# Performance work log

Hardware: AMD Instinct MI355X
Metric: run time of the kernel (lower is better)

The kernel has to match this reference:

```python
import jax, jax.numpy as jnp
import numpy as np

HID = 128      # hidden_dim
HEADS = 8      # num_heads
PHD = 16       # per_head_dim
NTYPES = 3     # num_edge_types
N = 50000      # num nodes
E = 250000     # edges per edge type


def setup_inputs() -> dict:
    key = jax.random.key(0)
    ks = jax.random.split(key, 8)
    x = jax.random.normal(ks[0], (N, HID), dtype=jnp.float32)
    adj0 = jax.random.randint(ks[1], (E, 2), 0, N)
    adj1 = jax.random.randint(ks[2], (E, 2), 0, N)
    adj2 = jax.random.randint(ks[3], (E, 2), 0, N)
    # weights stored [in, out] so application is x @ W (same math as torch Linear)
    Wq = jax.random.normal(ks[4], (NTYPES, HID, HEADS * PHD), dtype=jnp.float32) * 0.05
    Wk = jax.random.normal(ks[5], (NTYPES, HID, HEADS * PHD), dtype=jnp.float32) * 0.05
    Wm = jax.random.normal(ks[6], (NTYPES, 2 * HID, HEADS * PHD), dtype=jnp.float32) * 0.05
    bm = jax.random.normal(ks[7], (NTYPES, HEADS * PHD), dtype=jnp.float32) * 0.01
    return {"x": x, "adj0": adj0, "adj1": adj1, "adj2": adj2,
            "Wq": Wq, "Wk": Wk, "Wm": Wm, "bm": bm}


def reference(x, adj0, adj1, adj2, Wq, Wk, Wm, bm):
    scale = PHD ** (-0.5)
    n = x.shape[0]
    msgs, scores, tgts = [], [], []
    for t, adj in enumerate((adj0, adj1, adj2)):
        src_r = x[adj[:, 0]]                       # [E, HID]
        tgt_r = x[adj[:, 1]]                       # [E, HID]
        pair = jnp.concatenate([src_r, tgt_r], axis=1)      # [E, 2*HID]
        m = jax.nn.relu(pair @ Wm[t] + bm[t]).reshape(-1, HEADS, PHD)
        q = (tgt_r @ Wq[t]).reshape(-1, HEADS, PHD) * scale
        k = (src_r @ Wk[t]).reshape(-1, HEADS, PHD)
        s = jnp.einsum('ehd,ehd->eh', q, k)        # [E, HEADS]
        msgs.append(m); scores.append(s); tgts.append(adj[:, 1])
    all_m = jnp.concatenate(msgs, axis=0)          # [TE, HEADS, PHD]
    all_s = jnp.concatenate(scores, axis=0)        # [TE, HEADS]
    all_t = jnp.concatenate(tgts, axis=0)          # [TE]
    # segment log-softmax over edges grouped by target node
    smax = jax.ops.segment_max(all_s, all_t, num_segments=n)        # [N, HEADS]
    shifted = all_s - smax[all_t]
    sumexp = jax.ops.segment_sum(jnp.exp(shifted), all_t, num_segments=n)
    logZ = jnp.log(jnp.where(sumexp > 0, sumexp, 1.0))
    probs = jnp.exp(shifted - logZ[all_t])                          # [TE, HEADS]
    agg = jax.ops.segment_sum(probs[..., None] * all_m, all_t, num_segments=n)
    return agg.reshape(n, HEADS * PHD)
```

## Files before the change

### kernel.cpp

```cpp
#include <hip/hip_runtime.h>

#define HID 128
#define NE 250000
#define NT 3
#define NN 50000
#define CAP 48
#define PLANE (NN * 256)
#define GEMM_BLOCKS 391
#define EDGE_BLOCKS ((NT * NE + 255) / 256)

typedef unsigned int u32;
typedef unsigned short u16;
typedef __attribute__((ext_vector_type(8))) short short8;
typedef __attribute__((ext_vector_type(4))) float f32x4;

__device__ __forceinline__ u16 f2bf(float f) {
    u32 u = __float_as_uint(f);
    u += 0x7fffu + ((u >> 16) & 1u);
    return (u16)(u >> 16);
}
__device__ __forceinline__ float bflo(u32 u) { return __uint_as_float(u << 16); }
__device__ __forceinline__ float bfhi(u32 u) { return __uint_as_float(u & 0xffff0000u); }

__device__ __forceinline__ short8 pack8(const float4 a, const float4 b) {
    short8 r;
    r[0] = (short)f2bf(a.x); r[1] = (short)f2bf(a.y);
    r[2] = (short)f2bf(a.z); r[3] = (short)f2bf(a.w);
    r[4] = (short)f2bf(b.x); r[5] = (short)f2bf(b.y);
    r[6] = (short)f2bf(b.z); r[7] = (short)f2bf(b.w);
    return r;
}

__global__ __launch_bounds__(256)
void init_kernel(const float* __restrict__ Wq, const float* __restrict__ Wk,
                 const float* __restrict__ Wm,
                 u16* __restrict__ Wtb, u32* __restrict__ counts)
{
    const int b = blockIdx.x, tid = threadIdx.x;
    if (b < 768) {
        const int gid = b * 256 + tid;
        const int mat = gid >> 14;
        const int i   = gid & 16383;
        const int k   = i >> 7;
        const int n   = i & 127;
        const int t   = mat >> 2;
        const int m   = mat & 3;
        const float* src;
        if (m == 0)      src = Wq + (size_t)t * 16384;
        else if (m == 1) src = Wk + (size_t)t * 16384;
        else if (m == 2) src = Wm + (size_t)t * 32768;
        else             src = Wm + (size_t)t * 32768 + 16384;
        Wtb[(size_t)mat * 16384 + n * HID + k] = f2bf(src[i]);
    } else {
        const int gid = (b - 768) * 256 + tid;
        if (gid < NN / 4) {
            uint4 z; z.x = 0u; z.y = 0u; z.z = 0u; z.w = 0u;
            ((uint4*)counts)[gid] = z;
        }
    }
}

__global__ __launch_bounds__(256)
void big_kernel(const float* __restrict__ x, const u16* __restrict__ Wtb,
                const float* __restrict__ bm,
                const int* __restrict__ a0, const int* __restrict__ a1,
                const int* __restrict__ a2,
                u32* __restrict__ counts, u32* __restrict__ edata,
                u16* __restrict__ P)
{
    const int b = blockIdx.x;
    const int tid = threadIdx.x;

    if (b >= GEMM_BLOCKS) {
        const int gid = (b - GEMM_BLOCKS) * 256 + tid;
        if (gid < NT * NE) {
            const int t = gid / NE, e = gid - t * NE;
            const int* adj = (t == 0) ? a0 : (t == 1) ? a1 : a2;
            const int2 pr = ((const int2*)adj)[e];
            const u32 pos = atomicAdd(&counts[pr.y], 1u);
            if (pos < CAP)
                edata[(size_t)pr.y * CAP + pos] = (u32)pr.x | ((u32)t << 16);
        }
        return;
    }

    const int wave = tid >> 6, lane = tid & 63;
    const int lm = lane & 15, quad = lane >> 4;
    const int r0 = b * 128 + wave * 32;
    const int ar0 = min(r0 + lm,      NN - 1);
    const int ar1 = min(r0 + 16 + lm, NN - 1);

    short8 Xf0[4], Xf1[4];
    #pragma unroll
    for (int ki = 0; ki < 4; ++ki) {
        const float* xp0 = x + (size_t)ar0 * HID + ki * 32 + quad * 8;
        const float* xp1 = x + (size_t)ar1 * HID + ki * 32 + quad * 8;
        Xf0[ki] = pack8(*(const float4*)xp0, *(const float4*)(xp0 + 4));
        Xf1[ki] = pack8(*(const float4*)xp1, *(const float4*)(xp1 + 4));
    }

    for (int mat = 0; mat < 12; ++mat) {
        const int t = mat >> 2, m = mat & 3;
        const u16* Wf0 = Wtb + (size_t)mat * 16384 + lm * HID + quad * 8;

        f32x4 acc[8][2];
        #pragma unroll
        for (int ct = 0; ct < 8; ++ct) {
            acc[ct][0] = (f32x4){0.f, 0.f, 0.f, 0.f};
            acc[ct][1] = (f32x4){0.f, 0.f, 0.f, 0.f};
        }
        #pragma unroll
        for (int ki = 0; ki < 4; ++ki) {
            #pragma unroll
            for (int ct = 0; ct < 8; ++ct) {
                const short8 Wf = *(const short8*)(Wf0 + ct * 16 * HID + ki * 32);
                acc[ct][0] = __builtin_amdgcn_mfma_f32_16x16x32_bf16(Wf, Xf0[ki], acc[ct][0], 0, 0, 0);
                acc[ct][1] = __builtin_amdgcn_mfma_f32_16x16x32_bf16(Wf, Xf1[ki], acc[ct][1], 0, 0, 0);
            }
        }

        const int half = (m >= 2) ? 128 : 0;
        const int pidx = (m == 1 || m == 2) ? t : (3 + t);
        u16* Pd = P + (size_t)pidx * PLANE + half;
        #pragma unroll
        for (int ct = 0; ct < 8; ++ct) {
            const int oc = ct * 16 + quad * 4;
            float b0 = 0.f, b1 = 0.f, b2 = 0.f, b3 = 0.f;
            if (m == 3) {
                const float4 bv = *(const float4*)(bm + t * HID + oc);
                b0 = bv.x; b1 = bv.y; b2 = bv.z; b3 = bv.w;
            }
            #pragma unroll
            for (int nt = 0; nt < 2; ++nt) {
                const int node = r0 + nt * 16 + lm;
                if (node < NN) {
                    uint2 pk;
                    pk.x = (u32)f2bf(acc[ct][nt][0] + b0) | ((u32)f2bf(acc[ct][nt][1] + b1) << 16);
                    pk.y = (u32)f2bf(acc[ct][nt][2] + b2) | ((u32)f2bf(acc[ct][nt][3] + b3) << 16);
                    *(uint2*)(Pd + (size_t)node * 256 + oc) = pk;
                }
            }
        }
    }
}

__global__ __launch_bounds__(256)
void gather_kernel(const u16* __restrict__ P, const u32* __restrict__ counts,
                   const u32* __restrict__ edata, float* __restrict__ out)
{
    const int wave = threadIdx.x >> 6, lane = threadIdx.x & 63;
    const int node = blockIdx.x * 4 + wave;
    if (node >= NN) return;
    const int j0 = lane * 2;

    const int dg = min((int)__builtin_amdgcn_readfirstlane((int)counts[node]), CAP);
    const int idxs = (lane < CAP) ? (int)edata[(size_t)node * CAP + lane] : 0;

    float q0[NT], q1[NT], b0[NT], b1[NT];
    #pragma unroll
    for (int t = 0; t < NT; ++t) {
        const u16* qb = P + (size_t)(3 + t) * PLANE + (size_t)node * 256;
        const u32 qv = *(const u32*)(qb + j0);
        const u32 bv = *(const u32*)(qb + 128 + j0);
        q0[t] = bflo(qv) * 0.25f;
        q1[t] = bfhi(qv) * 0.25f;
        b0[t] = bflo(bv);
        b1[t] = bfhi(bv);
    }

    float acc0 = 0.f, acc1 = 0.f, den = 0.f;
    for (int e = 0; e < dg; e += 16) {
        u32 kv[16], av[16];
        int ty[16];
        #pragma unroll
        for (int u = 0; u < 16; ++u) {
            int w = __builtin_amdgcn_readlane(idxs, e + u);
            w = (e + u < dg) ? w : 0;
            w = __builtin_amdgcn_readfirstlane(w);
            const int tt = w >> 16, s = w & 0xffff;
            ty[u] = tt;
            const u16* ka = P + (size_t)tt * PLANE + (size_t)s * 256;
            kv[u] = *(const u32*)(ka + j0);
            av[u] = *(const u32*)(ka + 128 + j0);
        }
        #pragma unroll
        for (int u = 0; u < 16; ++u) {
            const int tt = ty[u];
            const float cq0 = (tt == 0) ? q0[0] : (tt == 1) ? q0[1] : q0[2];
            const float cq1 = (tt == 0) ? q1[0] : (tt == 1) ? q1[1] : q1[2];
            const float cb0 = (tt == 0) ? b0[0] : (tt == 1) ? b0[1] : b0[2];
            const float cb1 = (tt == 0) ? b1[0] : (tt == 1) ? b1[1] : b1[2];
            float d = cq0 * bflo(kv[u]) + cq1 * bfhi(kv[u]);
            d += __shfl_xor(d, 1);
            d += __shfl_xor(d, 2);
            d += __shfl_xor(d, 4);
            float ex = __expf(d);
            ex = (e + u < dg) ? ex : 0.f;
            den  += ex;
            acc0 += ex * fmaxf(bflo(av[u]) + cb0, 0.f);
            acc1 += ex * fmaxf(bfhi(av[u]) + cb1, 0.f);
        }
    }

    const float inv = den > 0.f ? 1.f / den : 0.f;
    float2 o;
    o.x = acc0 * inv;
    o.y = acc1 * inv;
    *(float2*)(out + (size_t)node * HID + j0) = o;
}

extern "C" void kernel_launch(void* const* d_in, const int* in_sizes, int n_in,
                              void* d_out, int out_size, void* d_ws, size_t ws_size,
                              hipStream_t stream)
{
    const float* x  = (const float*)d_in[0];
    const int* a0   = (const int*)d_in[1];
    const int* a1   = (const int*)d_in[2];
    const int* a2   = (const int*)d_in[3];
    const float* Wq = (const float*)d_in[4];
    const float* Wk = (const float*)d_in[5];
    const float* Wm = (const float*)d_in[6];
    const float* bm = (const float*)d_in[7];
    float* out = (float*)d_out;

    const size_t planeB = (size_t)PLANE * sizeof(u16);
    char* p = (char*)d_ws;
    u16* P      = (u16*)p;  p += 6 * planeB;
    u16* Wtb    = (u16*)p;  p += 393216;
    u32* counts = (u32*)p;  p += 200000;
    u32* edata  = (u32*)p;

    init_kernel<<<768 + 49, 256, 0, stream>>>(Wq, Wk, Wm, Wtb, counts);
    big_kernel<<<GEMM_BLOCKS + EDGE_BLOCKS, 256, 0, stream>>>(
        x, Wtb, bm, a0, a1, a2, counts, edata, P);
    gather_kernel<<<(NN + 3) / 4, 256, 0, stream>>>(P, counts, edata, out);
}
```

Baseline: 267.3 us.

## Split GEMM work across waves by weight matrix with 16-node blocks

Each GEMM block now handles 16 nodes instead of 128, and its four waves each compute three of the twelve weight matrices rather than every wave computing all twelve for its own 32 nodes. This takes the block count from 391 to 3125, which fills the GPU better and cuts per-wave register pressure, with launch bounds set to ask for 4 blocks per SM. In exchange, each x row is loaded and converted redundantly by all four waves, and each MFMA reuses a weight fragment across 16 nodes instead of 32, which doubles weight traffic per node. NN divides evenly by 16, so the bounds checks can be dropped.

New measurement: 331.9 us. 24.2% more time.

```diff
diff --git a/kernel.cpp b/kernel.cpp
--- a/kernel.cpp
+++ b/kernel.cpp
@@ -6,7 +6,7 @@
 #define NN 50000
 #define CAP 48
 #define PLANE (NN * 256)
-#define GEMM_BLOCKS 391
+#define GEMM_BLOCKS 3125
 #define EDGE_BLOCKS ((NT * NE + 255) / 256)
 
 typedef unsigned int u32;
@@ -60,7 +60,7 @@
     }
 }
 
-__global__ __launch_bounds__(256)
+__global__ __launch_bounds__(256, 4)
 void big_kernel(const float* __restrict__ x, const u16* __restrict__ Wtb,
                 const float* __restrict__ bm,
                 const int* __restrict__ a0, const int* __restrict__ a1,
@@ -86,42 +86,36 @@
 
     const int wave = tid >> 6, lane = tid & 63;
     const int lm = lane & 15, quad = lane >> 4;
-    const int r0 = b * 128 + wave * 32;
-    const int ar0 = min(r0 + lm,      NN - 1);
-    const int ar1 = min(r0 + 16 + lm, NN - 1);
-
-    short8 Xf0[4], Xf1[4];
+    const int node = b * 16 + lm;
+
+    short8 Xf[4];
     #pragma unroll
     for (int ki = 0; ki < 4; ++ki) {
-        const float* xp0 = x + (size_t)ar0 * HID + ki * 32 + quad * 8;
-        const float* xp1 = x + (size_t)ar1 * HID + ki * 32 + quad * 8;
-        Xf0[ki] = pack8(*(const float4*)xp0, *(const float4*)(xp0 + 4));
-        Xf1[ki] = pack8(*(const float4*)xp1, *(const float4*)(xp1 + 4));
-    }
-
-    for (int mat = 0; mat < 12; ++mat) {
+        const float* xp = x + (size_t)node * HID + ki * 32 + quad * 8;
+        Xf[ki] = pack8(*(const float4*)xp, *(const float4*)(xp + 4));
+    }
+
+    #pragma unroll 1
+    for (int i = 0; i < 3; ++i) {
+        const int mat = wave * 3 + i;
         const int t = mat >> 2, m = mat & 3;
         const u16* Wf0 = Wtb + (size_t)mat * 16384 + lm * HID + quad * 8;
 
-        f32x4 acc[8][2];
-        #pragma unroll
-        for (int ct = 0; ct < 8; ++ct) {
-            acc[ct][0] = (f32x4){0.f, 0.f, 0.f, 0.f};
-            acc[ct][1] = (f32x4){0.f, 0.f, 0.f, 0.f};
-        }
+        f32x4 acc[8];
+        #pragma unroll
+        for (int ct = 0; ct < 8; ++ct) acc[ct] = (f32x4){0.f, 0.f, 0.f, 0.f};
         #pragma unroll
         for (int ki = 0; ki < 4; ++ki) {
             #pragma unroll
             for (int ct = 0; ct < 8; ++ct) {
                 const short8 Wf = *(const short8*)(Wf0 + ct * 16 * HID + ki * 32);
-                acc[ct][0] = __builtin_amdgcn_mfma_f32_16x16x32_bf16(Wf, Xf0[ki], acc[ct][0], 0, 0, 0);
-                acc[ct][1] = __builtin_amdgcn_mfma_f32_16x16x32_bf16(Wf, Xf1[ki], acc[ct][1], 0, 0, 0);
+                acc[ct] = __builtin_amdgcn_mfma_f32_16x16x32_bf16(Wf, Xf[ki], acc[ct], 0, 0, 0);
             }
         }
 
         const int half = (m >= 2) ? 128 : 0;
         const int pidx = (m == 1 || m == 2) ? t : (3 + t);
-        u16* Pd = P + (size_t)pidx * PLANE + half;
+        u16* Pd = P + (size_t)pidx * PLANE + half + (size_t)node * 256;
         #pragma unroll
         for (int ct = 0; ct < 8; ++ct) {
             const int oc = ct * 16 + quad * 4;
@@ -130,16 +124,10 @@
                 const float4 bv = *(const float4*)(bm + t * HID + oc);
                 b0 = bv.x; b1 = bv.y; b2 = bv.z; b3 = bv.w;
             }
-            #pragma unroll
-            for (int nt = 0; nt < 2; ++nt) {
-                const int node = r0 + nt * 16 + lm;
-                if (node < NN) {
-                    uint2 pk;
-                    pk.x = (u32)f2bf(acc[ct][nt][0] + b0) | ((u32)f2bf(acc[ct][nt][1] + b1) << 16);
-                    pk.y = (u32)f2bf(acc[ct][nt][2] + b2) | ((u32)f2bf(acc[ct][nt][3] + b3) << 16);
-                    *(uint2*)(Pd + (size_t)node * 256 + oc) = pk;
-                }
-            }
+            uint2 pk;
+            pk.x = (u32)f2bf(acc[ct][0] + b0) | ((u32)f2bf(acc[ct][1] + b1) << 16);
+            pk.y = (u32)f2bf(acc[ct][2] + b2) | ((u32)f2bf(acc[ct][3] + b3) << 16);
+            *(uint2*)(Pd + oc) = pk;
         }
     }
 }
```

## Stage GEMM weight tiles in double-buffered swizzled LDS with register prefetch

Applied to the files above, without the earlier changes.

Each GEMM block now copies each 128x128 bf16 weight matrix into shared memory, using an XOR swizzle so bank conflicts are avoided, and the MFMA loop reads its weight fragments from LDS instead of global memory. The next matrix is prefetched into registers during the current matrix's compute and written to the other LDS buffer, followed by a barrier. This removes the redundant per-wave global and L2 traffic for weights, since four waves previously each reloaded every matrix. In exchange it adds 64KB of LDS per block, which may reduce occupancy, plus extra staging registers and one barrier per matrix. The edge-binning blocks launched from the same kernel also have to reserve this LDS allocation.

Measured after the change: 224.8 us. 1.19x faster.

```diff
diff --git a/kernel.cpp b/kernel.cpp
--- a/kernel.cpp
+++ b/kernel.cpp
@@ -68,6 +68,7 @@
                 u32* __restrict__ counts, u32* __restrict__ edata,
                 u16* __restrict__ P)
 {
+    __shared__ u16 Ws[2][128 * 128];
     const int b = blockIdx.x;
     const int tid = threadIdx.x;
 
@@ -99,9 +100,32 @@
         Xf1[ki] = pack8(*(const float4*)xp1, *(const float4*)(xp1 + 4));
     }
 
+    {
+        short8 stg[8];
+        #pragma unroll
+        for (int i = 0; i < 8; ++i)
+            stg[i] = *(const short8*)(Wtb + (i * 256 + tid) * 8);
+        #pragma unroll
+        for (int i = 0; i < 8; ++i) {
+            const int C = i * 256 + tid, r = C >> 4, s = C & 15;
+            *(short8*)&Ws[0][(r * 16 + (s ^ (r & 15))) * 8] = stg[i];
+        }
+    }
+    __syncthreads();
+
+    #pragma unroll 1
     for (int mat = 0; mat < 12; ++mat) {
+        const int cur = mat & 1;
         const int t = mat >> 2, m = mat & 3;
-        const u16* Wf0 = Wtb + (size_t)mat * 16384 + lm * HID + quad * 8;
+        const bool more = (mat < 11);
+
+        short8 stg[8];
+        if (more) {
+            const u16* Wn = Wtb + (size_t)(mat + 1) * 16384;
+            #pragma unroll
+            for (int i = 0; i < 8; ++i)
+                stg[i] = *(const short8*)(Wn + (i * 256 + tid) * 8);
+        }
 
         f32x4 acc[8][2];
         #pragma unroll
@@ -113,7 +137,8 @@
         for (int ki = 0; ki < 4; ++ki) {
             #pragma unroll
             for (int ct = 0; ct < 8; ++ct) {
-                const short8 Wf = *(const short8*)(Wf0 + ct * 16 * HID + ki * 32);
+                const short8 Wf = *(const short8*)
+                    &Ws[cur][(ct * 16 + lm) * 128 + (((ki * 4 + quad) ^ lm) * 8)];
                 acc[ct][0] = __builtin_amdgcn_mfma_f32_16x16x32_bf16(Wf, Xf0[ki], acc[ct][0], 0, 0, 0);
                 acc[ct][1] = __builtin_amdgcn_mfma_f32_16x16x32_bf16(Wf, Xf1[ki], acc[ct][1], 0, 0, 0);
             }
@@ -140,6 +165,16 @@
                     *(uint2*)(Pd + (size_t)node * 256 + oc) = pk;
                 }
             }
+        }
+
+        if (more) {
+            #pragma unroll
+            for (int i = 0; i < 8; ++i) {
+                const int C = i * 256 + tid, r = C >> 4, s = C & 15;
+                *(short8*)&Ws[cur ^ 1][(r * 16 + (s ^ (r & 15))) * 8] = stg[i];
+            }
+            asm volatile("s_waitcnt lgkmcnt(0)" ::: "memory");
+            __builtin_amdgcn_s_barrier();
         }
     }
 }
```
